# Kernel optimization log

Hardware: AMD Instinct MI355X
Metric: run time of the kernel (lower is better)

The kernel has to match this reference:

```python
import jax, jax.numpy as jnp
import numpy as np

B, T, F, H, S = 4096, 256, 64, 128, 32


def setup_inputs() -> dict:
    key = jax.random.key(0)
    ks = jax.random.split(key, 10)
    return {
        "x": jax.random.normal(ks[0], (B, T, F), jnp.float32),
        "static": jax.random.normal(ks[1], (B, S), jnp.float32),
        "hs0": jax.random.normal(ks[2], (B, H), jnp.float32),
        "cs0": jax.random.normal(ks[3], (B, H), jnp.float32),
        "W_ih": jax.random.normal(ks[4], (4 * H, F), jnp.float32) * 0.1,
        "W_hh": jax.random.normal(ks[5], (4 * H, H), jnp.float32) * 0.1,
        "b_ih": jax.random.normal(ks[6], (4 * H,), jnp.float32) * 0.1,
        "b_hh": jax.random.normal(ks[7], (4 * H,), jnp.float32) * 0.1,
        "W_lin": jax.random.normal(ks[8], (1, H + S), jnp.float32) * 0.1,
        "b_lin": jax.random.normal(ks[9], (1,), jnp.float32) * 0.1,
    }


def reference(x, static, hs0, cs0, W_ih, W_hh, b_ih, b_hh, W_lin, b_lin):
    # x: [B, T, F] -> time-major [T, B, F]; precompute input projections for all steps
    xs = jnp.swapaxes(x, 0, 1)
    px = jnp.einsum('tbf,gf->tbg', xs, W_ih) + b_ih  # [T, B, 4H]

    def step(carry, px_t):
        h, c = carry
        gates = px_t + h @ W_hh.T + b_hh  # [B, 4H]
        i, f, g, o = jnp.split(gates, 4, axis=-1)  # PyTorch LSTM gate order
        i = jax.nn.sigmoid(i)
        f = jax.nn.sigmoid(f)
        g = jnp.tanh(g)
        o = jax.nn.sigmoid(o)
        c = f * c + i * g
        h = o * jnp.tanh(c)
        return (h, c), None

    (h, c), _ = jax.lax.scan(step, (hs0, cs0), px)
    full = jnp.concatenate([h, static], axis=1)  # [B, H+S]
    return full @ W_lin.T + b_lin  # [B, 1]
```

## Files before the change

### kernel.cpp

```cpp
#include <hip/hip_runtime.h>
#include <hip/hip_bf16.h>

#define B_ 4096
#define T_ 256
#define F_ 64
#define H_ 128
#define S_ 32

typedef __attribute__((ext_vector_type(8))) short bf16x8;
typedef __attribute__((ext_vector_type(4))) float f32x4;

#define K1f (-1.4426950408889634f)
#define K2f (-2.8853900817779268f)

#define MF(A, B, C) __builtin_amdgcn_mfma_f32_16x16x32_bf16((A), (B), (C), 0, 0, 0)

__device__ __forceinline__ float bf2f(unsigned short u) {
    unsigned v = (unsigned)u << 16;
    return __builtin_bit_cast(float, v);
}
__device__ __forceinline__ short f2bs(float f) {
    return (short)__bfloat16_as_ushort(__float2bfloat16(f));
}

#define PHASE(HR, HW, XW, XN, TLD)                                               \
  {                                                                              \
    const char* hr_ = (const char*)(HR);                                         \
    bf16x8 a0 = *(const bf16x8*)(hr_ + fh0);                                     \
    bf16x8 a1 = *(const bf16x8*)(hr_ + fh1);                                     \
    bf16x8 a2 = *(const bf16x8*)(hr_ + fh2);                                     \
    bf16x8 a3 = *(const bf16x8*)(hr_ + fh3);                                     \
                    \
    { __hip_bfloat162 qx = __float22bfloat162_rn(xheld);                         \
      *(__hip_bfloat162*)((char*)(XW) + xws) = qx; }                             \
    xheld = *(const float2*)(gxs + (size_t)(TLD) * F_);                          \
                                          \
    f32x4 ac0 = sd0, ac1 = sd1, ac2 = sd2, ac3 = sd3;                            \
    ac0 = MF(wf[0][2], a0, ac0); ac1 = MF(wf[1][2], a0, ac1);                    \
    ac2 = MF(wf[2][2], a0, ac2); ac3 = MF(wf[3][2], a0, ac3);                    \
    ac0 = MF(wf[0][3], a1, ac0); ac1 = MF(wf[1][3], a1, ac1);                    \
    ac2 = MF(wf[2][3], a1, ac2); ac3 = MF(wf[3][3], a1, ac3);                    \
    ac0 = MF(wf[0][4], a2, ac0); ac1 = MF(wf[1][4], a2, ac1);                    \
    ac2 = MF(wf[2][4], a2, ac2); ac3 = MF(wf[3][4], a2, ac3);                    \
    ac0 = MF(wf[0][5], a3, ac0); ac1 = MF(wf[1][5], a3, ac1);                    \
    ac2 = MF(wf[2][5], a3, ac2); ac3 = MF(wf[3][5], a3, ac3);                    \
                                                 \
    float hn[4];                                                                 \
    _Pragma("unroll")                                                            \
    for (int q = 0; q < 4; ++q) {                                                \
      const float ei = __builtin_amdgcn_exp2f(__builtin_fmaf(ac0[q], K1f, bs0[q])); \
      const float i_ = __builtin_amdgcn_rcpf(1.0f + ei);                         \
      const float ef = __builtin_amdgcn_exp2f(__builtin_fmaf(ac1[q], K1f, bs1[q])); \
      const float f_ = __builtin_amdgcn_rcpf(1.0f + ef);                         \
      const float eg = __builtin_amdgcn_exp2f(__builtin_fmaf(ac2[q], K2f, btn[q])); \
      const float g_ = __builtin_fmaf(2.0f, __builtin_amdgcn_rcpf(1.0f + eg), -1.0f); \
      const float eo = __builtin_amdgcn_exp2f(__builtin_fmaf(ac3[q], K1f, bs3[q])); \
      const float o_ = __builtin_amdgcn_rcpf(1.0f + eo);                         \
      const float cn = __builtin_fmaf(f_, c[q], i_ * g_);                        \
      c[q] = cn;                                                                 \
      const float ec = __builtin_amdgcn_exp2f(cn * K2f);                         \
      const float th = __builtin_fmaf(2.0f, __builtin_amdgcn_rcpf(1.0f + ec), -1.0f); \
      hn[q] = o_ * th;                                                           \
    }                                                                            \
    { float2 p0; p0.x = hn[0]; p0.y = hn[1];                                     \
      float2 p1; p1.x = hn[2]; p1.y = hn[3];                                     \
      __hip_bfloat162 b01 = __float22bfloat162_rn(p0);                           \
      __hip_bfloat162 b23 = __float22bfloat162_rn(p1);                           \
      uint2 uv; uv.x = *(unsigned*)&b01; uv.y = *(unsigned*)&b23;                \
      *(uint2*)((char*)(HW) + hwb) = uv; }                                       \
              \
    { const char* xn_ = (const char*)(XN);                                       \
      bf16x8 nf0 = *(const bf16x8*)(xn_ + fx0);                                  \
      bf16x8 nf1 = *(const bf16x8*)(xn_ + fx1);                                  \
      sd0 = MF(wf[0][0], nf0, z4); sd1 = MF(wf[1][0], nf0, z4);                  \
      sd2 = MF(wf[2][0], nf0, z4); sd3 = MF(wf[3][0], nf0, z4);                  \
      sd0 = MF(wf[0][1], nf1, sd0); sd1 = MF(wf[1][1], nf1, sd1);                \
      sd2 = MF(wf[2][1], nf1, sd2); sd3 = MF(wf[3][1], nf1, sd3); }              \
    asm volatile("s_waitcnt lgkmcnt(0)" ::: "memory");                           \
    __builtin_amdgcn_s_barrier();                                                \
  }

__global__ __launch_bounds__(512, 2) void lstm_fused_kernel(
    const float* __restrict__ x,
    const float* __restrict__ statik,
    const float* __restrict__ hs0,
    const float* __restrict__ cs0,
    const float* __restrict__ W_ih,
    const float* __restrict__ W_hh,
    const float* __restrict__ b_ih,
    const float* __restrict__ b_hh,
    const float* __restrict__ W_lin,
    const float* __restrict__ b_lin,
    float* __restrict__ out)
{
    __shared__ __align__(16) unsigned short h_l[2][16 * 128];
    __shared__ __align__(16) unsigned short x_l[4][16 * 64];

    const int tid  = threadIdx.x;
    const int lane = tid & 63;
    const int w    = tid >> 6;
    const int b0   = blockIdx.x * 16;

    const int lrow = lane & 15;
    const int lkb  = lane >> 4;
    const int n0q  = w * 16 + lkb * 4;

    bf16x8 wf[4][6];
    #pragma unroll
    for (int g = 0; g < 4; ++g) {
        const int n = g * 128 + w * 16 + lrow;
        #pragma unroll
        for (int kt = 0; kt < 6; ++kt) {
            const int k0 = kt * 32 + lkb * 8;
            const float* src = (kt < 2) ? (W_ih + n * F_ + k0)
                                        : (W_hh + n * H_ + (k0 - 64));
            const float4 s0 = *(const float4*)(src);
            const float4 s1 = *(const float4*)(src + 4);
            bf16x8 v;
            v[0] = f2bs(s0.x); v[1] = f2bs(s0.y); v[2] = f2bs(s0.z); v[3] = f2bs(s0.w);
            v[4] = f2bs(s1.x); v[5] = f2bs(s1.y); v[6] = f2bs(s1.z); v[7] = f2bs(s1.w);
            wf[g][kt] = v;
        }
    }

    float bs0[4], bs1[4], btn[4], bs3[4];
    #pragma unroll
    for (int g = 0; g < 4; ++g) {
        const float4 bi = *(const float4*)(b_ih + g * 128 + n0q);
        const float4 bh = *(const float4*)(b_hh + g * 128 + n0q);
        const float bq[4] = {bi.x + bh.x, bi.y + bh.y, bi.z + bh.z, bi.w + bh.w};
        #pragma unroll
        for (int q = 0; q < 4; ++q) {
            if (g == 0)      bs0[q] = bq[q] * K1f;
            else if (g == 1) bs1[q] = bq[q] * K1f;
            else if (g == 2) btn[q] = bq[q] * K2f;
            else             bs3[q] = bq[q] * K1f;
        }
    }

    float c[4];
    {
        const float4 cv = *(const float4*)(cs0 + (size_t)(b0 + lrow) * H_ + n0q);
        c[0] = cv.x; c[1] = cv.y; c[2] = cv.z; c[3] = cv.w;
    }

    const int fsw = (lrow & 7) << 4;
    const int fx0 = lrow * 128 + ((lkb * 16) ^ fsw);
    const int fx1 = lrow * 128 + ((64 + lkb * 16) ^ fsw);
    const int fh0 = lrow * 256 + ((0   + lkb * 16) ^ fsw);
    const int fh1 = lrow * 256 + ((64  + lkb * 16) ^ fsw);
    const int fh2 = lrow * 256 + ((128 + lkb * 16) ^ fsw);
    const int fh3 = lrow * 256 + ((192 + lkb * 16) ^ fsw);
    const int hwb = lrow * 256 + ((n0q * 2) ^ fsw);

    const int srow = tid >> 5;
    const int scp  = tid & 31;
    const int ssw  = (srow & 7) << 4;
    const int xws  = srow * 128 + ((scp * 4) ^ ssw);

    const float* gxs = x + (size_t)(b0 + srow) * (T_ * F_) + scp * 2;
    float2 xheld;
    {
        const float* hp = hs0 + (size_t)(b0 + srow) * H_ + scp * 2;
        const float2 hv0 = *(const float2*)(hp);
        const float2 hv1 = *(const float2*)(hp + 64);
        __hip_bfloat162 q0 = __float22bfloat162_rn(hv0);
        __hip_bfloat162 q1 = __float22bfloat162_rn(hv1);
        *(__hip_bfloat162*)((char*)h_l[0] + srow * 256 + ((scp * 4) ^ ssw))       = q0;
        *(__hip_bfloat162*)((char*)h_l[0] + srow * 256 + ((128 + scp * 4) ^ ssw)) = q1;

        const float2 x0 = *(const float2*)(gxs);
        const float2 x1 = *(const float2*)(gxs + F_);
        __hip_bfloat162 qa = __float22bfloat162_rn(x0);
        __hip_bfloat162 qb = __float22bfloat162_rn(x1);
        *(__hip_bfloat162*)((char*)x_l[0] + xws) = qa;
        *(__hip_bfloat162*)((char*)x_l[1] + xws) = qb;
        xheld = *(const float2*)(gxs + 2 * F_);
    }
    __syncthreads();

    const f32x4 z4 = {0.0f, 0.0f, 0.0f, 0.0f};

    f32x4 sd0, sd1, sd2, sd3;
    {
        const char* xn_ = (const char*)x_l[0];
        bf16x8 nf0 = *(const bf16x8*)(xn_ + fx0);
        bf16x8 nf1 = *(const bf16x8*)(xn_ + fx1);
        sd0 = MF(wf[0][0], nf0, z4); sd1 = MF(wf[1][0], nf0, z4);
        sd2 = MF(wf[2][0], nf0, z4); sd3 = MF(wf[3][0], nf0, z4);
        sd0 = MF(wf[0][1], nf1, sd0); sd1 = MF(wf[1][1], nf1, sd1);
        sd2 = MF(wf[2][1], nf1, sd2); sd3 = MF(wf[3][1], nf1, sd3);
    }

    for (int t = 0; t < T_; t += 4) {
        const int t3 = (t + 3 < T_) ? t + 3 : T_ - 1;
        const int t4 = (t + 4 < T_) ? t + 4 : T_ - 1;
        const int t5 = (t + 5 < T_) ? t + 5 : T_ - 1;
        const int t6 = (t + 6 < T_) ? t + 6 : T_ - 1;
        PHASE(h_l[0], h_l[1], x_l[2], x_l[1], t3);
        PHASE(h_l[1], h_l[0], x_l[3], x_l[2], t4);
        PHASE(h_l[0], h_l[1], x_l[0], x_l[3], t5);
        PHASE(h_l[1], h_l[0], x_l[1], x_l[0], t6);
    }

    {
        const char* hf = (const char*)h_l[0];
        const float wl0 = W_lin[lane];
        const float wl1 = W_lin[64 + lane];
        const float wl2 = (lane < S_) ? W_lin[128 + lane] : 0.0f;
        const float bl  = b_lin[0];
        #pragma unroll
        for (int rr = 0; rr < 2; ++rr) {
            const int r  = w * 2 + rr;
            const int rs = (r & 7) << 4;
            const unsigned short h0 =
                *(const unsigned short*)(hf + r * 256 + ((2 * lane) ^ rs));
            const unsigned short h1 =
                *(const unsigned short*)(hf + r * 256 + ((128 + 2 * lane) ^ rs));
            float p = bf2f(h0) * wl0 + bf2f(h1) * wl1;
            if (lane < S_) p += statik[(size_t)(b0 + r) * S_ + lane] * wl2;
            #pragma unroll
            for (int m = 32; m > 0; m >>= 1) p += __shfl_xor(p, m, 64);
            if (lane == 0) out[b0 + r] = p + bl;
        }
    }
}

extern "C" void kernel_launch(void* const* d_in, const int* in_sizes, int n_in,
                              void* d_out, int out_size, void* d_ws, size_t ws_size,
                              hipStream_t stream) {
    const float* x     = (const float*)d_in[0];
    const float* st    = (const float*)d_in[1];
    const float* hs0   = (const float*)d_in[2];
    const float* cs0   = (const float*)d_in[3];
    const float* W_ih  = (const float*)d_in[4];
    const float* W_hh  = (const float*)d_in[5];
    const float* b_ih  = (const float*)d_in[6];
    const float* b_hh  = (const float*)d_in[7];
    const float* W_lin = (const float*)d_in[8];
    const float* b_lin = (const float*)d_in[9];
    float* out = (float*)d_out;

    lstm_fused_kernel<<<dim3(B_ / 16), dim3(512), 0, stream>>>(
        x, st, hs0, cs0, W_ih, W_hh, b_ih, b_hh, W_lin, b_lin, out);
}
```

Before: 228.6 us.

## Interleave gate MFMAs with activation math using sched_group_barrier

Reorders each LSTM step so each gate's MFMA chain is followed by the previous gate's sigmoid/tanh math, and places the next step's input-projection MFMAs before the output-gate activation. Explicit sched_group_barrier hints tell the compiler how to interleave DS reads, MFMA and VALU groups. The aim is to hide the transcendental latency on the serial recurrence path behind matrix-core work. Hand-specified group counts can mismatch the actual instruction mix and constrain the scheduler, which could lengthen the critical path.

```diff
diff --git a/kernel.cpp b/kernel.cpp
--- a/kernel.cpp
+++ b/kernel.cpp
@@ -14,6 +14,7 @@
 #define K2f (-2.8853900817779268f)
 
 #define MF(A, B, C) __builtin_amdgcn_mfma_f32_16x16x32_bf16((A), (B), (C), 0, 0, 0)
+#define SGB(m, n) __builtin_amdgcn_sched_group_barrier((m), (n), 0)
 
 __device__ __forceinline__ float bf2f(unsigned short u) {
     unsigned v = (unsigned)u << 16;
@@ -34,40 +35,35 @@
     { __hip_bfloat162 qx = __float22bfloat162_rn(xheld);                         \
       *(__hip_bfloat162*)((char*)(XW) + xws) = qx; }                             \
     xheld = *(const float2*)(gxs + (size_t)(TLD) * F_);                          \
-                                          \
-    f32x4 ac0 = sd0, ac1 = sd1, ac2 = sd2, ac3 = sd3;                            \
-    ac0 = MF(wf[0][2], a0, ac0); ac1 = MF(wf[1][2], a0, ac1);                    \
-    ac2 = MF(wf[2][2], a0, ac2); ac3 = MF(wf[3][2], a0, ac3);                    \
-    ac0 = MF(wf[0][3], a1, ac0); ac1 = MF(wf[1][3], a1, ac1);                    \
-    ac2 = MF(wf[2][3], a1, ac2); ac3 = MF(wf[3][3], a1, ac3);                    \
-    ac0 = MF(wf[0][4], a2, ac0); ac1 = MF(wf[1][4], a2, ac1);                    \
-    ac2 = MF(wf[2][4], a2, ac2); ac3 = MF(wf[3][4], a2, ac3);                    \
-    ac0 = MF(wf[0][5], a3, ac0); ac1 = MF(wf[1][5], a3, ac1);                    \
-    ac2 = MF(wf[2][5], a3, ac2); ac3 = MF(wf[3][5], a3, ac3);                    \
-                                                 \
-    float hn[4];                                                                 \
-    _Pragma("unroll")                                                            \
-    for (int q = 0; q < 4; ++q) {                                                \
-      const float ei = __builtin_amdgcn_exp2f(__builtin_fmaf(ac0[q], K1f, bs0[q])); \
-      const float i_ = __builtin_amdgcn_rcpf(1.0f + ei);                         \
-      const float ef = __builtin_amdgcn_exp2f(__builtin_fmaf(ac1[q], K1f, bs1[q])); \
-      const float f_ = __builtin_amdgcn_rcpf(1.0f + ef);                         \
-      const float eg = __builtin_amdgcn_exp2f(__builtin_fmaf(ac2[q], K2f, btn[q])); \
-      const float g_ = __builtin_fmaf(2.0f, __builtin_amdgcn_rcpf(1.0f + eg), -1.0f); \
-      const float eo = __builtin_amdgcn_exp2f(__builtin_fmaf(ac3[q], K1f, bs3[q])); \
-      const float o_ = __builtin_amdgcn_rcpf(1.0f + eo);                         \
-      const float cn = __builtin_fmaf(f_, c[q], i_ * g_);                        \
-      c[q] = cn;                                                                 \
-      const float ec = __builtin_amdgcn_exp2f(cn * K2f);                         \
-      const float th = __builtin_fmaf(2.0f, __builtin_amdgcn_rcpf(1.0f + ec), -1.0f); \
-      hn[q] = o_ * th;                                                           \
-    }                                                                            \
-    { float2 p0; p0.x = hn[0]; p0.y = hn[1];                                     \
-      float2 p1; p1.x = hn[2]; p1.y = hn[3];                                     \
-      __hip_bfloat162 b01 = __float22bfloat162_rn(p0);                           \
-      __hip_bfloat162 b23 = __float22bfloat162_rn(p1);                           \
-      uint2 uv; uv.x = *(unsigned*)&b01; uv.y = *(unsigned*)&b23;                \
-      *(uint2*)((char*)(HW) + hwb) = uv; }                                       \
+    float si[4], sf[4], sg[4], so[4];                                            \
+                                                                 \
+    f32x4 ac0 = sd0;                                                             \
+    ac0 = MF(wf[0][2], a0, ac0); ac0 = MF(wf[0][3], a1, ac0);                    \
+    ac0 = MF(wf[0][4], a2, ac0); ac0 = MF(wf[0][5], a3, ac0);                    \
+                                                                 \
+    f32x4 ac1 = sd1;                                                             \
+    ac1 = MF(wf[1][2], a0, ac1); ac1 = MF(wf[1][3], a1, ac1);                    \
+    ac1 = MF(wf[1][4], a2, ac1); ac1 = MF(wf[1][5], a3, ac1);                    \
+    _Pragma("unroll")                                                            \
+    for (int q = 0; q < 4; ++q)                                                  \
+      si[q] = __builtin_amdgcn_rcpf(1.0f +                                       \
+              __builtin_amdgcn_exp2f(__builtin_fmaf(ac0[q], K1f, bs0[q])));      \
+                                                                 \
+    f32x4 ac2 = sd2;                                                             \
+    ac2 = MF(wf[2][2], a0, ac2); ac2 = MF(wf[2][3], a1, ac2);                    \
+    ac2 = MF(wf[2][4], a2, ac2); ac2 = MF(wf[2][5], a3, ac2);                    \
+    _Pragma("unroll")                                                            \
+    for (int q = 0; q < 4; ++q)                                                  \
+      sf[q] = __builtin_amdgcn_rcpf(1.0f +                                       \
+              __builtin_amdgcn_exp2f(__builtin_fmaf(ac1[q], K1f, bs1[q])));      \
+                                                                 \
+    f32x4 ac3 = sd3;                                                             \
+    ac3 = MF(wf[3][2], a0, ac3); ac3 = MF(wf[3][3], a1, ac3);                    \
+    ac3 = MF(wf[3][4], a2, ac3); ac3 = MF(wf[3][5], a3, ac3);                    \
+    _Pragma("unroll")                                                            \
+    for (int q = 0; q < 4; ++q)                                                  \
+      sg[q] = __builtin_fmaf(2.0f, __builtin_amdgcn_rcpf(1.0f +                  \
+              __builtin_amdgcn_exp2f(__builtin_fmaf(ac2[q], K2f, btn[q]))), -1.0f); \
               \
     { const char* xn_ = (const char*)(XN);                                       \
       bf16x8 nf0 = *(const bf16x8*)(xn_ + fx0);                                  \
@@ -76,6 +72,38 @@
       sd2 = MF(wf[2][0], nf0, z4); sd3 = MF(wf[3][0], nf0, z4);                  \
       sd0 = MF(wf[0][1], nf1, sd0); sd1 = MF(wf[1][1], nf1, sd1);                \
       sd2 = MF(wf[2][1], nf1, sd2); sd3 = MF(wf[3][1], nf1, sd3); }              \
+    _Pragma("unroll")                                                            \
+    for (int q = 0; q < 4; ++q)                                                  \
+      so[q] = __builtin_amdgcn_rcpf(1.0f +                                       \
+              __builtin_amdgcn_exp2f(__builtin_fmaf(ac3[q], K1f, bs3[q])));      \
+                                \
+    float hn[4];                                                                 \
+    _Pragma("unroll")                                                            \
+    for (int q = 0; q < 4; ++q) {                                                \
+      const float cn = __builtin_fmaf(sf[q], c[q], si[q] * sg[q]);               \
+      c[q] = cn;                                                                 \
+      const float ec = __builtin_amdgcn_exp2f(cn * K2f);                         \
+      const float th = __builtin_fmaf(2.0f, __builtin_amdgcn_rcpf(1.0f + ec), -1.0f); \
+      hn[q] = so[q] * th;                                                        \
+    }                                                                            \
+    { float2 p0; p0.x = hn[0]; p0.y = hn[1];                                     \
+      float2 p1; p1.x = hn[2]; p1.y = hn[3];                                     \
+      __hip_bfloat162 b01 = __float22bfloat162_rn(p0);                           \
+      __hip_bfloat162 b23 = __float22bfloat162_rn(p1);                           \
+      uint2 uv; uv.x = *(unsigned*)&b01; uv.y = *(unsigned*)&b23;                \
+      *(uint2*)((char*)(HW) + hwb) = uv; }                                       \
+            \
+    SGB(0x100, 4);                                  \
+    SGB(0x8,   4);                                  \
+    SGB(0x8,   4);                                  \
+    SGB(0x2,  16);                                  \
+    SGB(0x8,   4);                                  \
+    SGB(0x2,  16);                                  \
+    SGB(0x8,   4);                                  \
+    SGB(0x2,  17);                                  \
+    SGB(0x100, 2);                                  \
+    SGB(0x8,   8);                                  \
+    SGB(0x2,  16);                                  \
     asm volatile("s_waitcnt lgkmcnt(0)" ::: "memory");                           \
     __builtin_amdgcn_s_barrier();                                                \
   }
```

Measured after the change: 293.1 us (median of 2 runs). 1.28x slower.

## Split LSTM step into two half-phases with single h buffer and staggered activations

Applied to the files above, without the earlier changes.

Replaces the double-buffered hidden state with one shared buffer. Each timestep is split into two barrier-separated halves: first the second-half recurrent MFMAs run and the lower waves compute activations; then the upper waves compute activations while everyone runs the next step's input seeds and first-half recurrent MFMAs. This lets the next step's matrix work start on the freshly written first half of h, overlapping activation math with MFMA work. The cost is two barriers per timestep instead of one, and it relies on strict ordering of which waves own which hidden columns.

```diff
diff --git a/kernel.cpp b/kernel.cpp
--- a/kernel.cpp
+++ b/kernel.cpp
@@ -23,62 +23,63 @@
     return (short)__bfloat16_as_ushort(__float2bfloat16(f));
 }
 
-#define PHASE(HR, HW, XW, XN, TLD)                                               \
-  {                                                                              \
-    const char* hr_ = (const char*)(HR);                                         \
-    bf16x8 a0 = *(const bf16x8*)(hr_ + fh0);                                     \
-    bf16x8 a1 = *(const bf16x8*)(hr_ + fh1);                                     \
-    bf16x8 a2 = *(const bf16x8*)(hr_ + fh2);                                     \
-    bf16x8 a3 = *(const bf16x8*)(hr_ + fh3);                                     \
-                    \
-    { __hip_bfloat162 qx = __float22bfloat162_rn(xheld);                         \
-      *(__hip_bfloat162*)((char*)(XW) + xws) = qx; }                             \
-    xheld = *(const float2*)(gxs + (size_t)(TLD) * F_);                          \
-                                          \
-    f32x4 ac0 = sd0, ac1 = sd1, ac2 = sd2, ac3 = sd3;                            \
-    ac0 = MF(wf[0][2], a0, ac0); ac1 = MF(wf[1][2], a0, ac1);                    \
-    ac2 = MF(wf[2][2], a0, ac2); ac3 = MF(wf[3][2], a0, ac3);                    \
-    ac0 = MF(wf[0][3], a1, ac0); ac1 = MF(wf[1][3], a1, ac1);                    \
-    ac2 = MF(wf[2][3], a1, ac2); ac3 = MF(wf[3][3], a1, ac3);                    \
-    ac0 = MF(wf[0][4], a2, ac0); ac1 = MF(wf[1][4], a2, ac1);                    \
-    ac2 = MF(wf[2][4], a2, ac2); ac3 = MF(wf[3][4], a2, ac3);                    \
-    ac0 = MF(wf[0][5], a3, ac0); ac1 = MF(wf[1][5], a3, ac1);                    \
-    ac2 = MF(wf[2][5], a3, ac2); ac3 = MF(wf[3][5], a3, ac3);                    \
-                                                 \
-    float hn[4];                                                                 \
-    _Pragma("unroll")                                                            \
-    for (int q = 0; q < 4; ++q) {                                                \
+#define BARRIER() do { asm volatile("s_waitcnt lgkmcnt(0)" ::: "memory"); \
+                       __builtin_amdgcn_s_barrier(); } while (0)
+
+#define DO_SEEDS(XOFF) { \
+    const char* xb_ = (const char*)x_l + (XOFF); \
+    bf16x8 nf0 = *(const bf16x8*)(xb_ + fx0); \
+    bf16x8 nf1 = *(const bf16x8*)(xb_ + fx1); \
+    ac0 = MF(wf[0][0], nf0, z4);  ac1 = MF(wf[1][0], nf0, z4); \
+    ac2 = MF(wf[2][0], nf0, z4);  ac3 = MF(wf[3][0], nf0, z4); \
+    ac0 = MF(wf[0][1], nf1, ac0); ac1 = MF(wf[1][1], nf1, ac1); \
+    ac2 = MF(wf[2][1], nf1, ac2); ac3 = MF(wf[3][1], nf1, ac3); }
+
+#define DO_M23() { \
+    bf16x8 a0_ = *(const bf16x8*)(hb + fh0); \
+    bf16x8 a1_ = *(const bf16x8*)(hb + fh1); \
+    ac0 = MF(wf[0][2], a0_, ac0); ac1 = MF(wf[1][2], a0_, ac1); \
+    ac2 = MF(wf[2][2], a0_, ac2); ac3 = MF(wf[3][2], a0_, ac3); \
+    ac0 = MF(wf[0][3], a1_, ac0); ac1 = MF(wf[1][3], a1_, ac1); \
+    ac2 = MF(wf[2][3], a1_, ac2); ac3 = MF(wf[3][3], a1_, ac3); }
+
+#define DO_M45() { \
+    bf16x8 a2_ = *(const bf16x8*)(hb + fh2); \
+    bf16x8 a3_ = *(const bf16x8*)(hb + fh3); \
+    ac0 = MF(wf[0][4], a2_, ac0); ac1 = MF(wf[1][4], a2_, ac1); \
+    ac2 = MF(wf[2][4], a2_, ac2); ac3 = MF(wf[3][4], a2_, ac3); \
+    ac0 = MF(wf[0][5], a3_, ac0); ac1 = MF(wf[1][5], a3_, ac1); \
+    ac2 = MF(wf[2][5], a3_, ac2); ac3 = MF(wf[3][5], a3_, ac3); }
+
+#define DO_ACT() { \
+    float hn[4]; \
+    _Pragma("unroll") \
+    for (int q = 0; q < 4; ++q) { \
       const float ei = __builtin_amdgcn_exp2f(__builtin_fmaf(ac0[q], K1f, bs0[q])); \
-      const float i_ = __builtin_amdgcn_rcpf(1.0f + ei);                         \
+      const float i_ = __builtin_amdgcn_rcpf(1.0f + ei); \
       const float ef = __builtin_amdgcn_exp2f(__builtin_fmaf(ac1[q], K1f, bs1[q])); \
-      const float f_ = __builtin_amdgcn_rcpf(1.0f + ef);                         \
+      const float f_ = __builtin_amdgcn_rcpf(1.0f + ef); \
       const float eg = __builtin_amdgcn_exp2f(__builtin_fmaf(ac2[q], K2f, btn[q])); \
       const float g_ = __builtin_fmaf(2.0f, __builtin_amdgcn_rcpf(1.0f + eg), -1.0f); \
       const float eo = __builtin_amdgcn_exp2f(__builtin_fmaf(ac3[q], K1f, bs3[q])); \
-      const float o_ = __builtin_amdgcn_rcpf(1.0f + eo);                         \
-      const float cn = __builtin_fmaf(f_, c[q], i_ * g_);                        \
-      c[q] = cn;                                                                 \
-      const float ec = __builtin_amdgcn_exp2f(cn * K2f);                         \
+      const float o_ = __builtin_amdgcn_rcpf(1.0f + eo); \
+      const float cn = __builtin_fmaf(f_, c[q], i_ * g_); \
+      c[q] = cn; \
+      const float ec = __builtin_amdgcn_exp2f(cn * K2f); \
       const float th = __builtin_fmaf(2.0f, __builtin_amdgcn_rcpf(1.0f + ec), -1.0f); \
-      hn[q] = o_ * th;                                                           \
-    }                                                                            \
-    { float2 p0; p0.x = hn[0]; p0.y = hn[1];                                     \
-      float2 p1; p1.x = hn[2]; p1.y = hn[3];                                     \
-      __hip_bfloat162 b01 = __float22bfloat162_rn(p0);                           \
-      __hip_bfloat162 b23 = __float22bfloat162_rn(p1);                           \
-      uint2 uv; uv.x = *(unsigned*)&b01; uv.y = *(unsigned*)&b23;                \
-      *(uint2*)((char*)(HW) + hwb) = uv; }                                       \
-              \
-    { const char* xn_ = (const char*)(XN);                                       \
-      bf16x8 nf0 = *(const bf16x8*)(xn_ + fx0);                                  \
-      bf16x8 nf1 = *(const bf16x8*)(xn_ + fx1);                                  \
-      sd0 = MF(wf[0][0], nf0, z4); sd1 = MF(wf[1][0], nf0, z4);                  \
-      sd2 = MF(wf[2][0], nf0, z4); sd3 = MF(wf[3][0], nf0, z4);                  \
-      sd0 = MF(wf[0][1], nf1, sd0); sd1 = MF(wf[1][1], nf1, sd1);                \
-      sd2 = MF(wf[2][1], nf1, sd2); sd3 = MF(wf[3][1], nf1, sd3); }              \
-    asm volatile("s_waitcnt lgkmcnt(0)" ::: "memory");                           \
-    __builtin_amdgcn_s_barrier();                                                \
-  }
+      hn[q] = o_ * th; \
+    } \
+    { float2 p0; p0.x = hn[0]; p0.y = hn[1]; \
+      float2 p1; p1.x = hn[2]; p1.y = hn[3]; \
+      __hip_bfloat162 b01 = __float22bfloat162_rn(p0); \
+      __hip_bfloat162 b23 = __float22bfloat162_rn(p1); \
+      uint2 uv; uv.x = *(unsigned*)&b01; uv.y = *(unsigned*)&b23; \
+      *(uint2*)((char*)h_l + hwb) = uv; } }
+
+#define DO_STAGE(XWOFF, TLD) { \
+    __hip_bfloat162 qx_ = __float22bfloat162_rn(xheld); \
+    *(__hip_bfloat162*)((char*)x_l + (XWOFF) + xws) = qx_; \
+    xheld = *(const float2*)(gxs + (size_t)(TLD) * F_); }
 
 __global__ __launch_bounds__(512, 2) void lstm_fused_kernel(
     const float* __restrict__ x,
@@ -93,12 +94,13 @@
     const float* __restrict__ b_lin,
     float* __restrict__ out)
 {
-    __shared__ __align__(16) unsigned short h_l[2][16 * 128];
-    __shared__ __align__(16) unsigned short x_l[4][16 * 64];
+    __shared__ __align__(16) unsigned short h_l[16 * 128];
+    __shared__ __align__(16) unsigned short x_l[4 * 16 * 64];
 
     const int tid  = threadIdx.x;
     const int lane = tid & 63;
     const int w    = tid >> 6;
+    const bool hi  = (w >= 4);
     const int b0   = blockIdx.x * 16;
 
     const int lrow = lane & 15;
@@ -152,6 +154,7 @@
     const int fh2 = lrow * 256 + ((128 + lkb * 16) ^ fsw);
     const int fh3 = lrow * 256 + ((192 + lkb * 16) ^ fsw);
     const int hwb = lrow * 256 + ((n0q * 2) ^ fsw);
+    const char* hb = (const char*)h_l;
 
     const int srow = tid >> 5;
     const int scp  = tid & 31;
@@ -166,45 +169,49 @@
         const float2 hv1 = *(const float2*)(hp + 64);
         __hip_bfloat162 q0 = __float22bfloat162_rn(hv0);
         __hip_bfloat162 q1 = __float22bfloat162_rn(hv1);
-        *(__hip_bfloat162*)((char*)h_l[0] + srow * 256 + ((scp * 4) ^ ssw))       = q0;
-        *(__hip_bfloat162*)((char*)h_l[0] + srow * 256 + ((128 + scp * 4) ^ ssw)) = q1;
+        *(__hip_bfloat162*)((char*)h_l + srow * 256 + ((scp * 4) ^ ssw))       = q0;
+        *(__hip_bfloat162*)((char*)h_l + srow * 256 + ((128 + scp * 4) ^ ssw)) = q1;
 
         const float2 x0 = *(const float2*)(gxs);
         const float2 x1 = *(const float2*)(gxs + F_);
         __hip_bfloat162 qa = __float22bfloat162_rn(x0);
         __hip_bfloat162 qb = __float22bfloat162_rn(x1);
-        *(__hip_bfloat162*)((char*)x_l[0] + xws) = qa;
-        *(__hip_bfloat162*)((char*)x_l[1] + xws) = qb;
+        *(__hip_bfloat162*)((char*)x_l + 0*2048 + xws) = qa;
+        *(__hip_bfloat162*)((char*)x_l + 1*2048 + xws) = qb;
         xheld = *(const float2*)(gxs + 2 * F_);
     }
     __syncthreads();
 
     const f32x4 z4 = {0.0f, 0.0f, 0.0f, 0.0f};
-
-    f32x4 sd0, sd1, sd2, sd3;
+    f32x4 ac0, ac1, ac2, ac3;
+
+    DO_SEEDS(0);
+    DO_M23();
+    DO_STAGE(2 * 2048, 3);
+    BARRIER();
+
+    for (int t = 0; t < T_ - 1; ++t) {
+        DO_M45();
+        if (!hi) { DO_ACT(); }
+        BARRIER();
+
+        const int s    = t + 1;
+        const int xro  = (s & 3) << 11;
+        const int xwo2 = ((s + 2) & 3) << 11;
+        const int tld  = (s + 3 < T_) ? s + 3 : T_ - 1;
+        if (hi) { DO_ACT(); }
+        DO_SEEDS(xro);
+        DO_M23();
+        DO_STAGE(xwo2, tld);
+        BARRIER();
+    }
+
+    DO_M45();
+    DO_ACT();
+    BARRIER();
+
     {
-        const char* xn_ = (const char*)x_l[0];
-        bf16x8 nf0 = *(const bf16x8*)(xn_ + fx0);
-        bf16x8 nf1 = *(const bf16x8*)(xn_ + fx1);
-        sd0 = MF(wf[0][0], nf0, z4); sd1 = MF(wf[1][0], nf0, z4);
-        sd2 = MF(wf[2][0], nf0, z4); sd3 = MF(wf[3][0], nf0, z4);
-        sd0 = MF(wf[0][1], nf1, sd0); sd1 = MF(wf[1][1], nf1, sd1);
-        sd2 = MF(wf[2][1], nf1, sd2); sd3 = MF(wf[3][1], nf1, sd3);
-    }
-
-    for (int t = 0; t < T_; t += 4) {
-        const int t3 = (t + 3 < T_) ? t + 3 : T_ - 1;
-        const int t4 = (t + 4 < T_) ? t + 4 : T_ - 1;
-        const int t5 = (t + 5 < T_) ? t + 5 : T_ - 1;
-        const int t6 = (t + 6 < T_) ? t + 6 : T_ - 1;
-        PHASE(h_l[0], h_l[1], x_l[2], x_l[1], t3);
-        PHASE(h_l[1], h_l[0], x_l[3], x_l[2], t4);
-        PHASE(h_l[0], h_l[1], x_l[0], x_l[3], t5);
-        PHASE(h_l[1], h_l[0], x_l[1], x_l[0], t6);
-    }
-
-    {
-        const char* hf = (const char*)h_l[0];
+        const char* hf = (const char*)h_l;
         const float wl0 = W_lin[lane];
         const float wl1 = W_lin[64 + lane];
         const float wl2 = (lane < S_) ? W_lin[128 + lane] : 0.0f;
```

Result: slower. 258.8 us (+13.2%).
